# Kernel tuning notes

Measured on AMD Instinct MI355X. Metric: run time of the kernel, lower is better.

The kernel has to match this reference:

```python
import jax, jax.numpy as jnp
import numpy as np

T, B, I, H = 2048, 32, 256, 512


def setup_inputs() -> dict:
    key = jax.random.key(0)
    ks = jax.random.split(key, 4)
    x = jax.random.normal(ks[0], (T, B, I), dtype=jnp.float32)
    time = jax.random.uniform(ks[1], (T, B, 1), dtype=jnp.float32)
    # LSTM gate weights, order [i, f, g, o]; gate input is concat([x_t, dt_t])
    W_ih = jax.random.normal(ks[2], (4 * H, I + 1), dtype=jnp.float32) / np.sqrt(I + 1)
    W_hh = jax.random.normal(ks[3], (4 * H, H), dtype=jnp.float32) / np.sqrt(H)
    b = jnp.zeros((4 * H,), dtype=jnp.float32)
    h0 = jnp.zeros((B, H), dtype=jnp.float32)
    c0 = jnp.zeros((B, H), dtype=jnp.float32)
    return {"x": x, "time": time, "W_ih": W_ih, "W_hh": W_hh, "b": b, "h0": h0, "c0": c0}


def reference(x, time, W_ih, W_hh, b, h0, c0):
    # Sequential LSTM over the leading (time-major) axis, matching the
    # python for-loop `for i in range(len(inputs)): out, state = cell(...)`.
    def step(carry, xt):
        h, c = carry
        x_t, t_t = xt                                    # [B,I], [B,1]
        inp = jnp.concatenate([x_t, t_t], axis=-1)       # [B, I+1]
        z = inp @ W_ih.T + h @ W_hh.T + b                # [B, 4H]
        i_g, f_g, g_g, o_g = jnp.split(z, 4, axis=-1)
        i_g = jax.nn.sigmoid(i_g)
        f_g = jax.nn.sigmoid(f_g)
        g_g = jnp.tanh(g_g)
        o_g = jax.nn.sigmoid(o_g)
        c_new = f_g * c + i_g * g_g
        h_new = o_g * jnp.tanh(c_new)
        return (h_new, c_new), h_new

    (h_T, c_T), outputs = jax.lax.scan(step, (h0, c0), (x, time))
    return outputs, h_T, c_T  # outputs: [T,B,H] == torch.stack(outputs)
```

## Files before the change

### kernel.cpp

```cpp
#include <hip/hip_runtime.h>

#define TS    2048
#define BTOT  32
#define IDIM  256
#define HDIM  512
#define GRPS  8
#define WPG   32
#define BPG   4
#define NTHR  256
#define KX    8
#define KT    24
#define SROW  520

typedef __attribute__((ext_vector_type(8))) short    bfrag;
typedef __attribute__((ext_vector_type(4))) float    facc;
typedef unsigned long long u64;

#define LD_A64(p)   __hip_atomic_load((p),  __ATOMIC_RELAXED, __HIP_MEMORY_SCOPE_AGENT)
#define ST_A64(p,v) __hip_atomic_store((p),(v),__ATOMIC_RELAXED, __HIP_MEMORY_SCOPE_AGENT)

__device__ __forceinline__ unsigned short f2bf(float f){
    unsigned u = __builtin_bit_cast(unsigned, f);
    u += 0x7FFFu + ((u >> 16) & 1u);
    return (unsigned short)(u >> 16);
}
__device__ __forceinline__ unsigned pack2(float a, float b){
    return (unsigned)f2bf(a) | ((unsigned)f2bf(b) << 16);
}

#define LSTM_STEP(Tt, XF, TPF)                                                              \
  do {                                                                                      \
                     \
    const u64* hsrc = hgrp + (size_t)((Tt) & 1) * 1024 + (size_t)tid * 4;                   \
    u64 w0 = LD_A64(hsrc + 0), w1 = LD_A64(hsrc + 1);                                       \
    u64 w2 = LD_A64(hsrc + 2), w3 = LD_A64(hsrc + 3);                                       \
    facc ze = {0.f,0.f,0.f,0.f}, zo = {0.f,0.f,0.f,0.f};                                    \
    _Pragma("unroll")                                                                       \
    for (int j = 0; j < KX; j += 2){                                                        \
      ze = __builtin_amdgcn_mfma_f32_16x16x32_bf16(XF[j],   breg[j],   ze, 0,0,0);          \
      zo = __builtin_amdgcn_mfma_f32_16x16x32_bf16(XF[j+1], breg[j+1], zo, 0,0,0);          \
    }                                                                                       \
    const unsigned want = (unsigned)(Tt) + 1u;                                              \
    while ((((unsigned)(w0 >> 32) != want) | ((unsigned)(w1 >> 32) != want) |               \
            ((unsigned)(w2 >> 32) != want) | ((unsigned)(w3 >> 32) != want)) != 0u){        \
      if ((unsigned)(w0 >> 32) != want) w0 = LD_A64(hsrc + 0);                              \
      if ((unsigned)(w1 >> 32) != want) w1 = LD_A64(hsrc + 1);                              \
      if ((unsigned)(w2 >> 32) != want) w2 = LD_A64(hsrc + 2);                              \
      if ((unsigned)(w3 >> 32) != want) w3 = LD_A64(hsrc + 3);                              \
    }                                                                                       \
    { uint4 pv; pv.x = (unsigned)w0; pv.y = (unsigned)w1;                                   \
      pv.z = (unsigned)w2; pv.w = (unsigned)w3;                                             \
      *reinterpret_cast<uint4*>(                                                            \
          reinterpret_cast<char*>(hstage) + sb * (SROW*2) + sw * 4) = pv; }                 \
    __syncthreads();                                                      \
    _Pragma("unroll")                                                                       \
    for (int j = 0; j < 16; j += 2){                                                        \
      const bfrag ha = *reinterpret_cast<const bfrag*>(&hstage[lb*SROW + j*32 + kgrp*8]);   \
      const bfrag hb = *reinterpret_cast<const bfrag*>(&hstage[lb*SROW + (j+1)*32 + kgrp*8]); \
      ze = __builtin_amdgcn_mfma_f32_16x16x32_bf16(ha, breg[KX+j],   ze, 0,0,0);            \
      zo = __builtin_amdgcn_mfma_f32_16x16x32_bf16(hb, breg[KX+j+1], zo, 0,0,0);            \
    }                                                                                       \
    const facc zz = ze + zo;                                                                \
    if (lane < 16){                \
      _Pragma("unroll")                                                                     \
      for (int q = 0; q < 4; ++q) zfull[wv][q][lane] = zz[q];                               \
    }                                                                                       \
    __syncthreads();                                                       \
    float hn0 = 0.f, hn1 = 0.f;                                                             \
    if (gth){                                                                               \
      float zg0[4], zg1[4];                                                                 \
      _Pragma("unroll")                                                                     \
      for (int gt = 0; gt < 4; ++gt){                                                       \
        zg0[gt] = zfull[gt][b][col0]     + bs2[gt][0] + wt2[gt][0] * (TPF);                 \
        zg1[gt] = zfull[gt][b][col0 + 1] + bs2[gt][1] + wt2[gt][1] * (TPF);                 \
      }                                                                                     \
      { const float ig = 1.f/(1.f+__expf(-zg0[0]));                                         \
        const float fg = 1.f/(1.f+__expf(-zg0[1]));                                         \
        const float gg = 1.f - 2.f/(__expf(2.f*zg0[2])+1.f);                                \
        const float og = 1.f/(1.f+__expf(-zg0[3]));                                         \
        creg0 = fg*creg0 + ig*gg;                                                           \
        hn0 = og*(1.f - 2.f/(__expf(2.f*creg0)+1.f)); }                                     \
      { const float ig = 1.f/(1.f+__expf(-zg1[0]));                                         \
        const float fg = 1.f/(1.f+__expf(-zg1[1]));                                         \
        const float gg = 1.f - 2.f/(__expf(2.f*zg1[2])+1.f);                                \
        const float og = 1.f/(1.f+__expf(-zg1[3]));                                         \
        creg1 = fg*creg1 + ig*gg;                                                           \
        hn1 = og*(1.f - 2.f/(__expf(2.f*creg1)+1.f)); }                                     \
      ST_A64(hgrp + (size_t)(((Tt)+1) & 1) * 1024 + b*256 + r*8 + cp,                       \
             ((u64)((unsigned)(Tt) + 2u) << 32) | (u64)pack2(hn0, hn1));                    \
    }                                                                                       \
                                                     \
    { const int tn = ((Tt)+2 < TS) ? ((Tt)+2) : (TS-1);                                     \
      if (ldr){                                                                             \
        _Pragma("unroll")                                                                   \
        for (int j = 0; j < KX; ++j){                                                       \
          const float4* p4 = reinterpret_cast<const float4*>(                               \
              x + ((size_t)tn*BTOT + lbg)*IDIM + j*32 + kgrp*8);                            \
          const float4 f0 = p4[0], f1 = p4[1];                                              \
          bfrag v;                                                                          \
          v[0]=(short)f2bf(f0.x); v[1]=(short)f2bf(f0.y);                                   \
          v[2]=(short)f2bf(f0.z); v[3]=(short)f2bf(f0.w);                                   \
          v[4]=(short)f2bf(f1.x); v[5]=(short)f2bf(f1.y);                                   \
          v[6]=(short)f2bf(f1.z); v[7]=(short)f2bf(f1.w);                                   \
          XF[j] = v;                                                                        \
        }                                                                                   \
      }                                                                                     \
      if (gth){                                                                             \
        (TPF) = tim[(size_t)tn*BTOT + bglob];                                               \
        *reinterpret_cast<float2*>(                                                         \
            &out[((size_t)(Tt)*BTOT + bglob)*HDIM + hcol0]) = make_float2(hn0, hn1);        \
        if ((Tt) == TS-1){                                                                  \
          float* hT = out + (size_t)TS*BTOT*HDIM;                                           \
          float* cT = hT + (size_t)BTOT*HDIM;                                               \
          *reinterpret_cast<float2*>(&hT[(size_t)bglob*HDIM + hcol0]) = make_float2(hn0, hn1); \
          *reinterpret_cast<float2*>(&cT[(size_t)bglob*HDIM + hcol0]) = make_float2(creg0, creg1); \
        }                                                                                   \
      }                                                                                     \
    }                                                                                       \
  } while(0)

__global__ __launch_bounds__(NTHR, 1) void lstm_grp(
    const float* __restrict__ x,
    const float* __restrict__ tim,
    const float* __restrict__ Wih,
    const float* __restrict__ Whh,
    const float* __restrict__ bias,
    const float* __restrict__ h0,
    const float* __restrict__ c0,
    float* __restrict__ out,
    u64* __restrict__ hbuf)
{
    const int tid = threadIdx.x, bid = blockIdx.x;
    const int g = bid & 7, r = bid >> 3;
    const int wv = tid >> 6, lane = tid & 63, l15 = lane & 15, kgrp = lane >> 4;

    __shared__ unsigned short hstage[BPG * SROW];
    __shared__ float zfull[4][4][16];

    u64* hgrp = hbuf + (size_t)g * 2048;

    bfrag breg[KT];
    {
        const int colg = wv * HDIM + r * 16 + l15;
        #pragma unroll
        for (int j = 0; j < KT; ++j){
            const float* src = (j < KX)
                ? (Wih + (size_t)colg * (IDIM + 1) + j * 32 + kgrp * 8)
                : (Whh + (size_t)colg * HDIM + (j - KX) * 32 + kgrp * 8);
            bfrag v;
            #pragma unroll
            for (int q = 0; q < 8; ++q) v[q] = (short)f2bf(src[q]);
            breg[j] = v;
        }
    }

    const bool gth = (tid < 32);
    const int b = (tid >> 3) & 3, cp = tid & 7, col0 = cp * 2;
    const int hcol0 = r * 16 + col0, bglob = g * BPG + b;
    float bs2[4][2], wt2[4][2];
    float creg0 = 0.f, creg1 = 0.f;
    if (gth){
        #pragma unroll
        for (int gt = 0; gt < 4; ++gt){
            const size_t cg = (size_t)gt * HDIM + hcol0;
            bs2[gt][0] = bias[cg];     bs2[gt][1] = bias[cg + 1];
            wt2[gt][0] = Wih[cg * (IDIM + 1) + IDIM];
            wt2[gt][1] = Wih[(cg + 1) * (IDIM + 1) + IDIM];
        }
        creg0 = c0[(size_t)bglob * HDIM + hcol0];
        creg1 = c0[(size_t)bglob * HDIM + hcol0 + 1];
        ST_A64(hgrp + 0 * 1024 + b * 256 + r * 8 + cp,
               (1ULL << 32) | (u64)pack2(h0[(size_t)bglob * HDIM + hcol0],
                                         h0[(size_t)bglob * HDIM + hcol0 + 1]));
    } else {
        #pragma unroll
        for (int gt = 0; gt < 4; ++gt){
            bs2[gt][0] = bs2[gt][1] = wt2[gt][0] = wt2[gt][1] = 0.f;
        }
    }

    const int sb = (tid * 4) >> 8;
    const int sw = (tid * 4) & 255;

    const bool ldr = (l15 < 4);
    const int lb = l15 & 3;
    const int lbg = g * BPG + lb;

    bfrag xe[KX], xo[KX];
    #pragma unroll
    for (int j = 0; j < KX; ++j){
        bfrag zv; 
        #pragma unroll
        for (int q = 0; q < 8; ++q) zv[q] = 0;
        xe[j] = zv; xo[j] = zv;
    }
    if (ldr){
        #pragma unroll
        for (int j = 0; j < KX; ++j){
            const float4* p0 = reinterpret_cast<const float4*>(
                x + ((size_t)0 * BTOT + lbg) * IDIM + j * 32 + kgrp * 8);
            const float4* p1 = reinterpret_cast<const float4*>(
                x + ((size_t)1 * BTOT + lbg) * IDIM + j * 32 + kgrp * 8);
            const float4 a0 = p0[0], a1 = p0[1], b0 = p1[0], b1 = p1[1];
            bfrag v;
            v[0]=(short)f2bf(a0.x); v[1]=(short)f2bf(a0.y);
            v[2]=(short)f2bf(a0.z); v[3]=(short)f2bf(a0.w);
            v[4]=(short)f2bf(a1.x); v[5]=(short)f2bf(a1.y);
            v[6]=(short)f2bf(a1.z); v[7]=(short)f2bf(a1.w);
            xe[j] = v;
            bfrag w;
            w[0]=(short)f2bf(b0.x); w[1]=(short)f2bf(b0.y);
            w[2]=(short)f2bf(b0.z); w[3]=(short)f2bf(b0.w);
            w[4]=(short)f2bf(b1.x); w[5]=(short)f2bf(b1.y);
            w[6]=(short)f2bf(b1.z); w[7]=(short)f2bf(b1.w);
            xo[j] = w;
        }
    }
    float tpf0 = 0.f, tpf1 = 0.f;
    if (gth){
        tpf0 = tim[(size_t)0 * BTOT + bglob];
        tpf1 = tim[(size_t)1 * BTOT + bglob];
    }

    for (int t = 0; t < TS; t += 2){
        LSTM_STEP(t,     xe, tpf0);
        LSTM_STEP(t + 1, xo, tpf1);
    }
}

extern "C" void kernel_launch(void* const* d_in, const int* in_sizes, int n_in,
                              void* d_out, int out_size, void* d_ws, size_t ws_size,
                              hipStream_t stream) {
    const float* x    = (const float*)d_in[0];
    const float* tim  = (const float*)d_in[1];
    const float* Wih  = (const float*)d_in[2];
    const float* Whh  = (const float*)d_in[3];
    const float* bias = (const float*)d_in[4];
    const float* h0   = (const float*)d_in[5];
    const float* c0   = (const float*)d_in[6];

    u64* hbuf = (u64*)d_ws;

    hipMemsetAsync(d_ws, 0, GRPS * 2 * 1024 * sizeof(u64), stream);

    lstm_grp<<<GRPS * WPG, NTHR, 0, stream>>>(x, tim, Wih, Whh, bias, h0, c0,
                                              (float*)d_out, hbuf);
}
```

Measured before the change: 6.785 ms.

## Interleave gate columns per wave and finish the LSTM cell with lane shuffles

Reorganizes the MFMA column mapping so each wave holds all four gates for four hidden columns. The cell nonlinearity is then computed with intra-wave shuffles, which removes the zfull shared-memory exchange and the second __syncthreads per step. The h staging buffer is double-buffered in LDS with an XOR swizzle, accumulation is spread over four independent chains, and the next step's h polling loads are issued early. Every lane now does activation work, and all x rows are loaded by all lanes; the trade is redundant x loads and shuffle overhead, plus a more delicate publication pattern.

```diff
diff --git a/kernel.cpp b/kernel.cpp
--- a/kernel.cpp
+++ b/kernel.cpp
@@ -6,14 +6,12 @@
 #define HDIM  512
 #define GRPS  8
 #define WPG   32
-#define BPG   4
 #define NTHR  256
 #define KX    8
 #define KT    24
-#define SROW  520
-
-typedef __attribute__((ext_vector_type(8))) short    bfrag;
-typedef __attribute__((ext_vector_type(4))) float    facc;
+
+typedef __attribute__((ext_vector_type(8))) short bfrag;
+typedef __attribute__((ext_vector_type(4))) float facc;
 typedef unsigned long long u64;
 
 #define LD_A64(p)   __hip_atomic_load((p),  __ATOMIC_RELAXED, __HIP_MEMORY_SCOPE_AGENT)
@@ -28,98 +26,107 @@
     return (unsigned)f2bf(a) | ((unsigned)f2bf(b) << 16);
 }
 
-#define LSTM_STEP(Tt, XF, TPF)                                                              \
-  do {                                                                                      \
-                     \
-    const u64* hsrc = hgrp + (size_t)((Tt) & 1) * 1024 + (size_t)tid * 4;                   \
-    u64 w0 = LD_A64(hsrc + 0), w1 = LD_A64(hsrc + 1);                                       \
-    u64 w2 = LD_A64(hsrc + 2), w3 = LD_A64(hsrc + 3);                                       \
-    facc ze = {0.f,0.f,0.f,0.f}, zo = {0.f,0.f,0.f,0.f};                                    \
-    _Pragma("unroll")                                                                       \
-    for (int j = 0; j < KX; j += 2){                                                        \
-      ze = __builtin_amdgcn_mfma_f32_16x16x32_bf16(XF[j],   breg[j],   ze, 0,0,0);          \
-      zo = __builtin_amdgcn_mfma_f32_16x16x32_bf16(XF[j+1], breg[j+1], zo, 0,0,0);          \
-    }                                                                                       \
-    const unsigned want = (unsigned)(Tt) + 1u;                                              \
-    while ((((unsigned)(w0 >> 32) != want) | ((unsigned)(w1 >> 32) != want) |               \
-            ((unsigned)(w2 >> 32) != want) | ((unsigned)(w3 >> 32) != want)) != 0u){        \
-      if ((unsigned)(w0 >> 32) != want) w0 = LD_A64(hsrc + 0);                              \
-      if ((unsigned)(w1 >> 32) != want) w1 = LD_A64(hsrc + 1);                              \
-      if ((unsigned)(w2 >> 32) != want) w2 = LD_A64(hsrc + 2);                              \
-      if ((unsigned)(w3 >> 32) != want) w3 = LD_A64(hsrc + 3);                              \
-    }                                                                                       \
-    { uint4 pv; pv.x = (unsigned)w0; pv.y = (unsigned)w1;                                   \
-      pv.z = (unsigned)w2; pv.w = (unsigned)w3;                                             \
-      *reinterpret_cast<uint4*>(                                                            \
-          reinterpret_cast<char*>(hstage) + sb * (SROW*2) + sw * 4) = pv; }                 \
-    __syncthreads();                                                      \
-    _Pragma("unroll")                                                                       \
-    for (int j = 0; j < 16; j += 2){                                                        \
-      const bfrag ha = *reinterpret_cast<const bfrag*>(&hstage[lb*SROW + j*32 + kgrp*8]);   \
-      const bfrag hb = *reinterpret_cast<const bfrag*>(&hstage[lb*SROW + (j+1)*32 + kgrp*8]); \
-      ze = __builtin_amdgcn_mfma_f32_16x16x32_bf16(ha, breg[KX+j],   ze, 0,0,0);            \
-      zo = __builtin_amdgcn_mfma_f32_16x16x32_bf16(hb, breg[KX+j+1], zo, 0,0,0);            \
-    }                                                                                       \
-    const facc zz = ze + zo;                                                                \
-    if (lane < 16){                \
-      _Pragma("unroll")                                                                     \
-      for (int q = 0; q < 4; ++q) zfull[wv][q][lane] = zz[q];                               \
-    }                                                                                       \
-    __syncthreads();                                                       \
-    float hn0 = 0.f, hn1 = 0.f;                                                             \
-    if (gth){                                                                               \
-      float zg0[4], zg1[4];                                                                 \
-      _Pragma("unroll")                                                                     \
-      for (int gt = 0; gt < 4; ++gt){                                                       \
-        zg0[gt] = zfull[gt][b][col0]     + bs2[gt][0] + wt2[gt][0] * (TPF);                 \
-        zg1[gt] = zfull[gt][b][col0 + 1] + bs2[gt][1] + wt2[gt][1] * (TPF);                 \
-      }                                                                                     \
-      { const float ig = 1.f/(1.f+__expf(-zg0[0]));                                         \
-        const float fg = 1.f/(1.f+__expf(-zg0[1]));                                         \
-        const float gg = 1.f - 2.f/(__expf(2.f*zg0[2])+1.f);                                \
-        const float og = 1.f/(1.f+__expf(-zg0[3]));                                         \
-        creg0 = fg*creg0 + ig*gg;                                                           \
-        hn0 = og*(1.f - 2.f/(__expf(2.f*creg0)+1.f)); }                                     \
-      { const float ig = 1.f/(1.f+__expf(-zg1[0]));                                         \
-        const float fg = 1.f/(1.f+__expf(-zg1[1]));                                         \
-        const float gg = 1.f - 2.f/(__expf(2.f*zg1[2])+1.f);                                \
-        const float og = 1.f/(1.f+__expf(-zg1[3]));                                         \
-        creg1 = fg*creg1 + ig*gg;                                                           \
-        hn1 = og*(1.f - 2.f/(__expf(2.f*creg1)+1.f)); }                                     \
-      ST_A64(hgrp + (size_t)(((Tt)+1) & 1) * 1024 + b*256 + r*8 + cp,                       \
-             ((u64)((unsigned)(Tt) + 2u) << 32) | (u64)pack2(hn0, hn1));                    \
-    }                                                                                       \
-                                                     \
-    { const int tn = ((Tt)+2 < TS) ? ((Tt)+2) : (TS-1);                                     \
-      if (ldr){                                                                             \
-        _Pragma("unroll")                                                                   \
-        for (int j = 0; j < KX; ++j){                                                       \
-          const float4* p4 = reinterpret_cast<const float4*>(                               \
-              x + ((size_t)tn*BTOT + lbg)*IDIM + j*32 + kgrp*8);                            \
-          const float4 f0 = p4[0], f1 = p4[1];                                              \
-          bfrag v;                                                                          \
-          v[0]=(short)f2bf(f0.x); v[1]=(short)f2bf(f0.y);                                   \
-          v[2]=(short)f2bf(f0.z); v[3]=(short)f2bf(f0.w);                                   \
-          v[4]=(short)f2bf(f1.x); v[5]=(short)f2bf(f1.y);                                   \
-          v[6]=(short)f2bf(f1.z); v[7]=(short)f2bf(f1.w);                                   \
-          XF[j] = v;                                                                        \
-        }                                                                                   \
-      }                                                                                     \
-      if (gth){                                                                             \
-        (TPF) = tim[(size_t)tn*BTOT + bglob];                                               \
-        *reinterpret_cast<float2*>(                                                         \
-            &out[((size_t)(Tt)*BTOT + bglob)*HDIM + hcol0]) = make_float2(hn0, hn1);        \
-        if ((Tt) == TS-1){                                                                  \
-          float* hT = out + (size_t)TS*BTOT*HDIM;                                           \
-          float* cT = hT + (size_t)BTOT*HDIM;                                               \
-          *reinterpret_cast<float2*>(&hT[(size_t)bglob*HDIM + hcol0]) = make_float2(hn0, hn1); \
-          *reinterpret_cast<float2*>(&cT[(size_t)bglob*HDIM + hcol0]) = make_float2(creg0, creg1); \
-        }                                                                                   \
-      }                                                                                     \
-    }                                                                                       \
+
+#define XREFILL(XF_, tn_) do{                                                   \
+    _Pragma("unroll")                                                           \
+    for (int j = 0; j < KX; ++j){                                               \
+      const float4* p4 = reinterpret_cast<const float4*>(                       \
+          x + ((size_t)(tn_)*BTOT + xrow)*IDIM + j*32 + kgrp*8);                \
+      const float4 f0 = p4[0], f1 = p4[1];                                      \
+      bfrag v;                                                                  \
+      v[0]=(short)f2bf(f0.x); v[1]=(short)f2bf(f0.y);                           \
+      v[2]=(short)f2bf(f0.z); v[3]=(short)f2bf(f0.w);                           \
+      v[4]=(short)f2bf(f1.x); v[5]=(short)f2bf(f1.y);                           \
+      v[6]=(short)f2bf(f1.z); v[7]=(short)f2bf(f1.w);                           \
+      XF_[j] = v;                                                               \
+    }                                                                           \
+  }while(0)
+
+#define LSTM_STEP(Tt, XF_, TPF_)                                                \
+  do {                                                                          \
+    facc acc[4];                                                                \
+    _Pragma("unroll")                                                           \
+    for (int q = 0; q < 4; ++q) acc[q] = (facc){0.f,0.f,0.f,0.f};               \
+           \
+    _Pragma("unroll")                                                           \
+    for (int j = 0; j < KX; ++j)                                                \
+      acc[j & 3] = __builtin_amdgcn_mfma_f32_16x16x32_bf16(XF_[j], breg[j],     \
+                                                           acc[j & 3], 0,0,0); \
+         \
+    { const unsigned want = (unsigned)(Tt) + 1u;                                \
+      while ((((unsigned)(w0 >> 32) != want) | ((unsigned)(w1 >> 32) != want) | \
+              ((unsigned)(w2 >> 32) != want) | ((unsigned)(w3 >> 32) != want))  \
+             != 0u){                                                            \
+        if ((unsigned)(w0 >> 32) != want) w0 = LD_A64(hsrc + 0);                \
+        if ((unsigned)(w1 >> 32) != want) w1 = LD_A64(hsrc + 1);                \
+        if ((unsigned)(w2 >> 32) != want) w2 = LD_A64(hsrc + 2);                \
+        if ((unsigned)(w3 >> 32) != want) w3 = LD_A64(hsrc + 3);                \
+      } }                                                                       \
+                 \
+    { uint4 pv; pv.x = (unsigned)w0; pv.y = (unsigned)w1;                       \
+      pv.z = (unsigned)w2; pv.w = (unsigned)w3;                                 \
+      *reinterpret_cast<uint4*>(                                                \
+          reinterpret_cast<char*>(&hstage[(Tt) & 1][0][0]) + stoff) = pv; }     \
+    __syncthreads();                                     \
+           \
+    { const char* hbase =                                                       \
+          reinterpret_cast<const char*>(&hstage[(Tt) & 1][0][0]);               \
+      _Pragma("unroll")                                                         \
+      for (int jj = 0; jj < 16; ++jj){                                          \
+        const bfrag hf = *reinterpret_cast<const bfrag*>(                       \
+            hbase + (hrdbase ^ (jj * 64)));                                     \
+        acc[jj & 3] = __builtin_amdgcn_mfma_f32_16x16x32_bf16(hf, breg[KX+jj],  \
+                                                              acc[jj & 3],     \
+                                                              0,0,0);          \
+      } }                                                                       \
+    const facc zz = (acc[0] + acc[1]) + (acc[2] + acc[3]);                      \
+         \
+    float zq = zz[0];                                                           \
+    zq = (kgrp == 1) ? zz[1] : zq;                                              \
+    zq = (kgrp == 2) ? zz[2] : zq;                                              \
+    zq = (kgrp == 3) ? zz[3] : zq;                                              \
+    zq += bsL + wtL * (TPF_);                                                   \
+                  \
+    const float zI = __shfl(zq, qb + 0);                                        \
+    const float zF = __shfl(zq, qb + 1);                                        \
+    const float zG = __shfl(zq, qb + 2);                                        \
+    const float zO = __shfl(zq, qb + 3);                                        \
+    const float ig = 1.f / (1.f + __expf(-zI));                                 \
+    const float fg = 1.f / (1.f + __expf(-zF));                                 \
+    const float gg = 1.f - 2.f / (__expf(2.f * zG) + 1.f);                      \
+    const float og = 1.f / (1.f + __expf(-zO));                                 \
+    creg = fg * creg + ig * gg;                                                 \
+    const float hn = og * (1.f - 2.f / (__expf(2.f * creg) + 1.f));             \
+    const float hnR = __shfl_xor(hn, 4);               \
+    if (pubL)                                                                   \
+      ST_A64(hgrp + (size_t)(((Tt) + 1) & 1) * 1024 + kgrp * 256 + (hcol >> 1), \
+             ((u64)((unsigned)(Tt) + 2u) << 32) | (u64)pack2(hn, hnR));         \
+         \
+    { const int tn = ((Tt) + 2 < TS) ? ((Tt) + 2) : (TS - 1);                   \
+      hsrc = hgrp + (size_t)(((Tt) + 1) & 1) * 1024 + (size_t)tid * 4;          \
+      w0 = LD_A64(hsrc + 0); w1 = LD_A64(hsrc + 1);                             \
+      w2 = LD_A64(hsrc + 2); w3 = LD_A64(hsrc + 3);                             \
+      XREFILL(XF_, tn);                                                         \
+      (TPF_) = tim[(size_t)tn * BTOT + bglob];                                  \
+      if (pubL)                                                                 \
+        *reinterpret_cast<float2*>(                                             \
+            &out[((size_t)(Tt) * BTOT + bglob) * HDIM + hcol]) =                \
+            make_float2(hn, hnR);                                               \
+      if ((Tt) == TS - 1){                                                      \
+        const float cR = __shfl_xor(creg, 4);                                   \
+        if (pubL){                                                              \
+          float* hT = out + (size_t)TS * BTOT * HDIM;                           \
+          float* cT = hT + (size_t)BTOT * HDIM;                                 \
+          *reinterpret_cast<float2*>(&hT[(size_t)bglob * HDIM + hcol]) =        \
+              make_float2(hn, hnR);                                             \
+          *reinterpret_cast<float2*>(&cT[(size_t)bglob * HDIM + hcol]) =        \
+              make_float2(creg, cR);                                            \
+        }                                                                       \
+      }                                                                         \
+    }                                                                           \
   } while(0)
 
-__global__ __launch_bounds__(NTHR, 1) void lstm_grp(
+__global__ __launch_bounds__(NTHR, 1) void lstm_bfly(
     const float* __restrict__ x,
     const float* __restrict__ tim,
     const float* __restrict__ Wih,
@@ -134,97 +141,57 @@
     const int g = bid & 7, r = bid >> 3;
     const int wv = tid >> 6, lane = tid & 63, l15 = lane & 15, kgrp = lane >> 4;
 
-    __shared__ unsigned short hstage[BPG * SROW];
-    __shared__ float zfull[4][4][16];
+    const int gq   = l15 & 3;
+    const int c4   = l15 >> 2;
+    const int hcol = r * 16 + wv * 4 + c4;
+    const int bglob = g * 4 + kgrp;
+    const int xrow  = g * 4 + gq;
+    const int qb    = lane & ~3;
+    const bool pubL = (l15 == 0) || (l15 == 8);
+
+    __shared__ unsigned short hstage[2][4][512];
 
     u64* hgrp = hbuf + (size_t)g * 2048;
 
     bfrag breg[KT];
-    {
-        const int colg = wv * HDIM + r * 16 + l15;
+    const int colg = gq * HDIM + hcol;
+    #pragma unroll
+    for (int j = 0; j < KT; ++j){
+        const float* src = (j < KX)
+            ? (Wih + (size_t)colg * (IDIM + 1) + j * 32 + kgrp * 8)
+            : (Whh + (size_t)colg * HDIM + (j - KX) * 32 + kgrp * 8);
+        bfrag v;
         #pragma unroll
-        for (int j = 0; j < KT; ++j){
-            const float* src = (j < KX)
-                ? (Wih + (size_t)colg * (IDIM + 1) + j * 32 + kgrp * 8)
-                : (Whh + (size_t)colg * HDIM + (j - KX) * 32 + kgrp * 8);
-            bfrag v;
-            #pragma unroll
-            for (int q = 0; q < 8; ++q) v[q] = (short)f2bf(src[q]);
-            breg[j] = v;
-        }
+        for (int q = 0; q < 8; ++q) v[q] = (short)f2bf(src[q]);
+        breg[j] = v;
     }
 
-    const bool gth = (tid < 32);
-    const int b = (tid >> 3) & 3, cp = tid & 7, col0 = cp * 2;
-    const int hcol0 = r * 16 + col0, bglob = g * BPG + b;
-    float bs2[4][2], wt2[4][2];
-    float creg0 = 0.f, creg1 = 0.f;
-    if (gth){
-        #pragma unroll
-        for (int gt = 0; gt < 4; ++gt){
-            const size_t cg = (size_t)gt * HDIM + hcol0;
-            bs2[gt][0] = bias[cg];     bs2[gt][1] = bias[cg + 1];
-            wt2[gt][0] = Wih[cg * (IDIM + 1) + IDIM];
-            wt2[gt][1] = Wih[(cg + 1) * (IDIM + 1) + IDIM];
-        }
-        creg0 = c0[(size_t)bglob * HDIM + hcol0];
-        creg1 = c0[(size_t)bglob * HDIM + hcol0 + 1];
-        ST_A64(hgrp + 0 * 1024 + b * 256 + r * 8 + cp,
-               (1ULL << 32) | (u64)pack2(h0[(size_t)bglob * HDIM + hcol0],
-                                         h0[(size_t)bglob * HDIM + hcol0 + 1]));
-    } else {
-        #pragma unroll
-        for (int gt = 0; gt < 4; ++gt){
-            bs2[gt][0] = bs2[gt][1] = wt2[gt][0] = wt2[gt][1] = 0.f;
-        }
-    }
-
-    const int sb = (tid * 4) >> 8;
-    const int sw = (tid * 4) & 255;
-
-    const bool ldr = (l15 < 4);
-    const int lb = l15 & 3;
-    const int lbg = g * BPG + lb;
+    const float bsL = bias[colg];
+    const float wtL = Wih[(size_t)colg * (IDIM + 1) + IDIM];
+    float creg = c0[(size_t)bglob * HDIM + hcol];
+
+    if (pubL)
+        ST_A64(hgrp + 0 * 1024 + kgrp * 256 + (hcol >> 1),
+               (1ULL << 32) | (u64)pack2(h0[(size_t)bglob * HDIM + hcol],
+                                         h0[(size_t)bglob * HDIM + hcol + 1]));
+
+    const int swb   = tid >> 6;
+    const int stoff = swb * 1024 + (((tid & 63) * 16) ^ (swb << 5));
+    const int hrdbase = gq * 1024 + ((kgrp * 16) ^ (gq << 5));
+
+    const u64* hsrc = hgrp + (size_t)tid * 4;
+    u64 w0 = LD_A64(hsrc + 0), w1 = LD_A64(hsrc + 1);
+    u64 w2 = LD_A64(hsrc + 2), w3 = LD_A64(hsrc + 3);
 
     bfrag xe[KX], xo[KX];
-    #pragma unroll
-    for (int j = 0; j < KX; ++j){
-        bfrag zv; 
-        #pragma unroll
-        for (int q = 0; q < 8; ++q) zv[q] = 0;
-        xe[j] = zv; xo[j] = zv;
-    }
-    if (ldr){
-        #pragma unroll
-        for (int j = 0; j < KX; ++j){
-            const float4* p0 = reinterpret_cast<const float4*>(
-                x + ((size_t)0 * BTOT + lbg) * IDIM + j * 32 + kgrp * 8);
-            const float4* p1 = reinterpret_cast<const float4*>(
-                x + ((size_t)1 * BTOT + lbg) * IDIM + j * 32 + kgrp * 8);
-            const float4 a0 = p0[0], a1 = p0[1], b0 = p1[0], b1 = p1[1];
-            bfrag v;
-            v[0]=(short)f2bf(a0.x); v[1]=(short)f2bf(a0.y);
-            v[2]=(short)f2bf(a0.z); v[3]=(short)f2bf(a0.w);
-            v[4]=(short)f2bf(a1.x); v[5]=(short)f2bf(a1.y);
-            v[6]=(short)f2bf(a1.z); v[7]=(short)f2bf(a1.w);
-            xe[j] = v;
-            bfrag w;
-            w[0]=(short)f2bf(b0.x); w[1]=(short)f2bf(b0.y);
-            w[2]=(short)f2bf(b0.z); w[3]=(short)f2bf(b0.w);
-            w[4]=(short)f2bf(b1.x); w[5]=(short)f2bf(b1.y);
-            w[6]=(short)f2bf(b1.z); w[7]=(short)f2bf(b1.w);
-            xo[j] = w;
-        }
-    }
-    float tpf0 = 0.f, tpf1 = 0.f;
-    if (gth){
-        tpf0 = tim[(size_t)0 * BTOT + bglob];
-        tpf1 = tim[(size_t)1 * BTOT + bglob];
-    }
+    XREFILL(xe, 0);
+    XREFILL(xo, 1);
+    float tpe = tim[(size_t)0 * BTOT + bglob];
+    float tpo = tim[(size_t)1 * BTOT + bglob];
 
     for (int t = 0; t < TS; t += 2){
-        LSTM_STEP(t,     xe, tpf0);
-        LSTM_STEP(t + 1, xo, tpf1);
+        LSTM_STEP(t,     xe, tpe);
+        LSTM_STEP(t + 1, xo, tpo);
     }
 }
 
@@ -243,6 +210,6 @@
 
     hipMemsetAsync(d_ws, 0, GRPS * 2 * 1024 * sizeof(u64), stream);
 
-    lstm_grp<<<GRPS * WPG, NTHR, 0, stream>>>(x, tim, Wih, Whh, bias, h0, c0,
-                                              (float*)d_out, hbuf);
-}
+    lstm_bfly<<<GRPS * WPG, NTHR, 0, stream>>>(x, tim, Wih, Whh, bias, h0, c0,
+                                               (float*)d_out, hbuf);
+}
```

Measured after the change: 10.87 ms. 1.6x slower.
